# Optimization experiments

Measured on AMD Instinct MI355X. Metric: run time of the kernel, lower is better.

The kernel has to match this reference:

```python
import jax, jax.numpy as jnp
import numpy as np

N_NODES = 512      # num_nodes (seq_len for LSTM, also output side length)
B = 64             # graph batch -> total nodes = B * N_NODES
T = B * N_NODES    # 32768 total nodes
E = 1048576        # edges before self-loops
D_IN = 128
H = 128
L = 2              # lstm layers


def setup_inputs() -> dict:
    key = jax.random.key(0)
    ks = jax.random.split(key, 12)
    x = jax.random.normal(ks[0], (T, D_IN), dtype=jnp.float32)
    edge_index = jax.random.randint(ks[1], (2, E), 0, T, dtype=jnp.int64)
    edge_weight = jax.random.uniform(ks[2], (E,), dtype=jnp.float32)
    batch = jax.random.randint(ks[3], (T,), 0, B, dtype=jnp.int64)
    s = 1.0 / np.sqrt(H)
    W_gcn = jax.random.normal(ks[4], (D_IN, H), dtype=jnp.float32) * s
    b_gcn = jnp.zeros((H,), dtype=jnp.float32)
    w_ih = jax.random.uniform(ks[5], (L, 4 * H, H), minval=-s, maxval=s, dtype=jnp.float32)
    w_hh = jax.random.uniform(ks[6], (L, 4 * H, H), minval=-s, maxval=s, dtype=jnp.float32)
    b_ih = jax.random.uniform(ks[7], (L, 4 * H), minval=-s, maxval=s, dtype=jnp.float32)
    b_hh = jax.random.uniform(ks[8], (L, 4 * H), minval=-s, maxval=s, dtype=jnp.float32)
    fc_w = jax.random.uniform(ks[9], (N_NODES * N_NODES, H), minval=-s, maxval=s, dtype=jnp.float32)
    fc_b = jax.random.uniform(ks[10], (N_NODES * N_NODES,), minval=-s, maxval=s, dtype=jnp.float32)
    return {"x": x, "edge_index": edge_index, "edge_weight": edge_weight, "batch": batch,
            "W_gcn": W_gcn, "b_gcn": b_gcn, "w_ih": w_ih, "w_hh": w_hh,
            "b_ih": b_ih, "b_hh": b_hh, "fc_w": fc_w, "fc_b": fc_b}


def _gcn_conv(x, edge_index, edge_weight, W, b):
    # PyG GCNConv with edge weights: add self-loops (w=1), symmetric norm, then aggregate.
    n = x.shape[0]
    loop = jnp.arange(n, dtype=edge_index.dtype)
    src = jnp.concatenate([edge_index[0], loop])
    dst = jnp.concatenate([edge_index[1], loop])
    w = jnp.concatenate([edge_weight, jnp.ones((n,), dtype=edge_weight.dtype)])
    deg = jax.ops.segment_sum(w, dst, num_segments=n)
    dinv = jnp.where(deg > 0, jax.lax.rsqrt(jnp.maximum(deg, 1e-30)), 0.0)
    norm = dinv[src] * w * dinv[dst]                  # [E+n]
    xw = x @ W                                        # [n, H]
    msg = norm[:, None] * xw[src]                     # gather + scale
    out = jax.ops.segment_sum(msg, dst, num_segments=n)  # scatter-add
    return out + b


def _lstm_layer(xs, wih, whh, bih, bhh):
    # xs: [S, B, H] time-major; torch gate order i,f,g,o.
    h0 = jnp.zeros((xs.shape[1], whh.shape[1]), dtype=xs.dtype)
    c0 = jnp.zeros_like(h0)
    def step(carry, xt):
        h, c = carry
        gates = xt @ wih.T + h @ whh.T + bih + bhh
        i, f, g, o = jnp.split(gates, 4, axis=-1)
        c = jax.nn.sigmoid(f) * c + jax.nn.sigmoid(i) * jnp.tanh(g)
        h = jax.nn.sigmoid(o) * jnp.tanh(c)
        return (h, c), h
    _, hs = jax.lax.scan(step, (h0, c0), xs)
    return hs


def reference(x, edge_index, edge_weight, batch, W_gcn, b_gcn, w_ih, w_hh, b_ih, b_hh, fc_w, fc_b):
    h = _gcn_conv(x, edge_index, edge_weight, W_gcn, b_gcn)   # [T, H]
    # split into chunks of num_nodes and stack -> [B, N_NODES, H]
    h = h.reshape(B, N_NODES, H)
    xs = jnp.transpose(h, (1, 0, 2))                           # [S, B, H]
    for l in range(L):
        xs = _lstm_layer(xs, w_ih[l], w_hh[l], b_ih[l], b_hh[l])
    last = xs[-1]                                              # [B, H]
    out = last @ fc_w.T + fc_b                                 # [B, N_NODES^2]
    return out.reshape(N_NODES, -1)
```

## Files before the change

### kernel.cpp

```cpp
#include <hip/hip_runtime.h>

#define TNODES 32768
#define NEDGE  1048576
#define HD     128
#define NG     512
#define NB     64
#define SEQ    512
#define FCN    262144

__global__ __launch_bounds__(256) void k_deg(const int* __restrict__ ei,
                                             const float* __restrict__ ew,
                                             float* __restrict__ deg,
                                             int* __restrict__ cnt) {
    int e = blockIdx.x * 256 + threadIdx.x;
    int d = ei[NEDGE + e];
    atomicAdd(&deg[d], ew[e]);
    atomicAdd(&cnt[d], 1);
}

__global__ __launch_bounds__(256) void k_dinv(float* __restrict__ deg) {
    int n = blockIdx.x * 256 + threadIdx.x;
    deg[n] = rsqrtf(deg[n] + 1.0f);
}

__global__ __launch_bounds__(1024) void k_scan(const int* __restrict__ cnt,
                                               int* __restrict__ offs) {
    __shared__ int sums[1024];
    int t = threadIdx.x;
    int base = t * 32;
    int local[32];
    int s = 0;
    #pragma unroll
    for (int j = 0; j < 32; ++j) { local[j] = s; s += cnt[base + j]; }
    sums[t] = s;
    __syncthreads();
    for (int off = 1; off < 1024; off <<= 1) {
        int v = sums[t];
        int u = (t >= off) ? sums[t - off] : 0;
        __syncthreads();
        sums[t] = v + u;
        __syncthreads();
    }
    int baseSum = (t == 0) ? 0 : sums[t - 1];
    #pragma unroll
    for (int j = 0; j < 32; ++j) offs[base + j] = baseSum + local[j];
    if (t == 1023) offs[TNODES] = sums[1023];
}

__global__ __launch_bounds__(256) void k_fill(const int* __restrict__ ei,
                                              const float* __restrict__ ew,
                                              const float* __restrict__ dinv,
                                              const int* __restrict__ offs,
                                              int* __restrict__ cursor,
                                              int* __restrict__ csrc,
                                              float* __restrict__ ca) {
    int e = blockIdx.x * 256 + threadIdx.x;
    int s = ei[e];
    int d = ei[NEDGE + e];
    int p = offs[d] + atomicAdd(&cursor[d], 1);
    csrc[p] = s;
    ca[p] = ew[e] * dinv[s];
}

__global__ __launch_bounds__(256) void k_transpose(const float* __restrict__ W,
                                                   float* __restrict__ Wt) {
    int t = blockIdx.x * 256 + threadIdx.x;
    int c = t >> 7, k = t & 127;
    Wt[t] = W[k * HD + c];
}

#define GS 140
__global__ __launch_bounds__(256) void k_gemm_bt(const float* __restrict__ A,
                                                 const float* __restrict__ Bt,
                                                 const float* __restrict__ b1,
                                                 const float* __restrict__ b2,
                                                 float* __restrict__ C, int G) {
    __shared__ __align__(16) float As[64 * GS];
    __shared__ __align__(16) float Bs[64 * GS];
    int r0 = blockIdx.x * 64;
    int g0 = blockIdx.y * 64;
    int tid = threadIdx.x;
    #pragma unroll
    for (int it = 0; it < 8; ++it) {
        int idx = tid + 256 * it;
        int r = idx >> 5, c4 = idx & 31;
        float4 va = ((const float4*)(A + (size_t)(r0 + r) * HD))[c4];
        *((float4*)&As[r * GS + c4 * 4]) = va;
        float4 vb = ((const float4*)(Bt + (size_t)(g0 + r) * HD))[c4];
        *((float4*)&Bs[r * GS + c4 * 4]) = vb;
    }
    __syncthreads();
    int i = tid >> 4;
    int j = tid & 15;
    float acc[4][4];
    #pragma unroll
    for (int a = 0; a < 4; ++a)
        #pragma unroll
        for (int b = 0; b < 4; ++b) acc[a][b] = 0.f;
    #pragma unroll 8
    for (int k4 = 0; k4 < 32; ++k4) {
        float4 av[4], bv[4];
        #pragma unroll
        for (int mi = 0; mi < 4; ++mi)
            av[mi] = *((const float4*)&As[(i + 16 * mi) * GS + k4 * 4]);
        #pragma unroll
        for (int ni = 0; ni < 4; ++ni)
            bv[ni] = *((const float4*)&Bs[(j + 16 * ni) * GS + k4 * 4]);
        #pragma unroll
        for (int mi = 0; mi < 4; ++mi)
            #pragma unroll
            for (int ni = 0; ni < 4; ++ni)
                acc[mi][ni] += (av[mi].x * bv[ni].x + av[mi].y * bv[ni].y) +
                               (av[mi].z * bv[ni].z + av[mi].w * bv[ni].w);
    }
    #pragma unroll
    for (int mi = 0; mi < 4; ++mi)
        #pragma unroll
        for (int ni = 0; ni < 4; ++ni) {
            int g = g0 + j + 16 * ni;
            float bias = (b1 ? b1[g] : 0.f) + (b2 ? b2[g] : 0.f);
            C[(size_t)(r0 + i + 16 * mi) * G + g] = acc[mi][ni] + bias;
        }
}

__global__ __launch_bounds__(128) void k_agg(const int* __restrict__ offs,
                                             const int* __restrict__ csrc,
                                             const float* __restrict__ ca,
                                             const float* __restrict__ xw,
                                             const float* __restrict__ dinv,
                                             const float* __restrict__ bg,
                                             float* __restrict__ hg) {
    int d = blockIdx.x;
    int t = threadIdx.x;
    int beg = offs[d], end = offs[d + 1];
    float acc = 0.f;
    int e = beg;
    for (; e + 3 < end; e += 4) {
        int s0 = csrc[e], s1 = csrc[e + 1], s2 = csrc[e + 2], s3 = csrc[e + 3];
        float a0 = ca[e], a1 = ca[e + 1], a2 = ca[e + 2], a3 = ca[e + 3];
        acc += a0 * xw[(size_t)s0 * HD + t];
        acc += a1 * xw[(size_t)s1 * HD + t];
        acc += a2 * xw[(size_t)s2 * HD + t];
        acc += a3 * xw[(size_t)s3 * HD + t];
    }
    for (; e < end; ++e) acc += ca[e] * xw[(size_t)csrc[e] * HD + t];
    float di = dinv[d];
    hg[(size_t)d * HD + t] = di * acc + di * di * xw[(size_t)d * HD + t] + bg[t];
}

__device__ __forceinline__ float sigm(float x) { return 1.f / (1.f + __expf(-x)); }
__device__ __forceinline__ float tanh_s(float x) {
    float e = __expf(-2.f * fabsf(x));
    float t = (1.f - e) / (1.f + e);
    return copysignf(t, x);
}

__global__ __launch_bounds__(512, 2) void k_lstm(const float* __restrict__ P,
                                                 const float* __restrict__ whh,
                                                 float* __restrict__ Hout,
                                                 float* __restrict__ lastOut) {
    __shared__ __align__(16) float h_sh[HD];
    __shared__ float g_sh[NG];
    int b = blockIdx.x, t = threadIdx.x;
    float4 w[32];
    #pragma unroll
    for (int kk = 0; kk < 32; ++kk) w[kk] = ((const float4*)(whh + (size_t)t * HD))[kk];
    float c = 0.f;
    if (t < HD) h_sh[t] = 0.f;
    __syncthreads();
    const float* Pb = P + (size_t)b * SEQ * NG;
    for (int s = 0; s < SEQ; ++s) {
        float p = Pb[(size_t)s * NG + t];
        float a0 = 0.f, a1 = 0.f, a2 = 0.f, a3 = 0.f;
        #pragma unroll
        for (int kk = 0; kk < 32; ++kk) {
            float4 h4 = ((const float4*)h_sh)[kk];
            a0 += w[kk].x * h4.x;
            a1 += w[kk].y * h4.y;
            a2 += w[kk].z * h4.z;
            a3 += w[kk].w * h4.w;
        }
        float raw = ((a0 + a1) + (a2 + a3)) + p;
        float act = (t >= 256 && t < 384) ? tanh_s(raw) : sigm(raw);
        g_sh[t] = act;
        __syncthreads();
        if (t < HD) {
            float i_ = g_sh[t], f_ = g_sh[HD + t], gg = g_sh[2 * HD + t], o_ = g_sh[3 * HD + t];
            c = f_ * c + i_ * gg;
            float h = o_ * tanh_s(c);
            h_sh[t] = h;
            if (Hout) Hout[((size_t)b * SEQ + s) * HD + t] = h;
            if (lastOut && s == SEQ - 1) lastOut[b * HD + t] = h;
        }
        __syncthreads();
    }
}

__global__ __launch_bounds__(256) void k_fc(const float* __restrict__ last,
                                            const float* __restrict__ fcw,
                                            const float* __restrict__ fcb,
                                            float* __restrict__ out) {
    __shared__ __align__(16) float l_sh[NB * HD];
    int tid = threadIdx.x;
    #pragma unroll
    for (int it = 0; it < 32; ++it) l_sh[tid + 256 * it] = last[tid + 256 * it];
    __syncthreads();
    int i = blockIdx.x * 256 + tid;
    const float4* wrow = (const float4*)(fcw + (size_t)i * HD);
    float acc[NB];
    #pragma unroll
    for (int b = 0; b < NB; ++b) acc[b] = 0.f;
    for (int k4 = 0; k4 < 32; ++k4) {
        float4 w4 = wrow[k4];
        #pragma unroll
        for (int b = 0; b < NB; ++b) {
            float4 l4 = ((const float4*)(l_sh + b * HD))[k4];
            acc[b] += (w4.x * l4.x + w4.y * l4.y) + (w4.z * l4.z + w4.w * l4.w);
        }
    }
    float bias = fcb[i];
    #pragma unroll
    for (int b = 0; b < NB; ++b) out[(size_t)b * FCN + i] = acc[b] + bias;
}

extern "C" void kernel_launch(void* const* d_in, const int* in_sizes, int n_in,
                              void* d_out, int out_size, void* d_ws, size_t ws_size,
                              hipStream_t stream) {
    const float* x   = (const float*)d_in[0];
    const int*   ei  = (const int*)d_in[1];
    const float* ew  = (const float*)d_in[2];
    const float* Wg  = (const float*)d_in[4];
    const float* bg  = (const float*)d_in[5];
    const float* wih = (const float*)d_in[6];
    const float* whh = (const float*)d_in[7];
    const float* bih = (const float*)d_in[8];
    const float* bhh = (const float*)d_in[9];
    const float* fcw = (const float*)d_in[10];
    const float* fcb = (const float*)d_in[11];
    float* out = (float*)d_out;

    float* ws = (float*)d_ws;
    float* deg    = ws;
    int*   cnt    = (int*)(ws + 32768);
    int*   cursor = (int*)(ws + 65536);
    int*   offs   = (int*)(ws + 98304);
    int*   csrc   = (int*)(ws + 131136);
    float* ca     = ws + 1179712;
    float* Wt     = ws + 2228288;
    float* xw     = ws + 2244672;
    float* hg     = ws + 6438976;
    float* H0     = ws + 10633280;
    float* lastb  = ws + 14827584;
    float* P      = ws + 14835776;

    hipMemsetAsync(d_ws, 0, 3 * 32768 * sizeof(float), stream);

    k_deg<<<NEDGE / 256, 256, 0, stream>>>(ei, ew, deg, cnt);
    k_dinv<<<TNODES / 256, 256, 0, stream>>>(deg);
    k_scan<<<1, 1024, 0, stream>>>(cnt, offs);
    k_fill<<<NEDGE / 256, 256, 0, stream>>>(ei, ew, deg, offs, cursor, csrc, ca);
    k_transpose<<<64, 256, 0, stream>>>(Wg, Wt);
    k_gemm_bt<<<dim3(TNODES / 64, HD / 64), 256, 0, stream>>>(x, Wt, nullptr, nullptr, xw, HD);
    k_agg<<<TNODES, 128, 0, stream>>>(offs, csrc, ca, xw, deg, bg, hg);

    k_gemm_bt<<<dim3(TNODES / 64, NG / 64), 256, 0, stream>>>(hg, wih, bih, bhh, P, NG);
    k_lstm<<<NB, 512, 0, stream>>>(P, whh, H0, nullptr);
    k_gemm_bt<<<dim3(TNODES / 64, NG / 64), 256, 0, stream>>>(H0, wih + 65536, bih + 512, bhh + 512, P, NG);
    k_lstm<<<NB, 512, 0, stream>>>(P, whh + 65536, nullptr, lastb);

    k_fc<<<FCN / 256, 256, 0, stream>>>(lastb, fcw, fcb, out);
}
```

Baseline: 1.705 ms.

## Restructure LSTM recurrence: two gate rows per thread, readlane broadcast of h

The LSTM kernel now runs 256 threads per block, and each thread holds two rows of the recurrent weight matrix in registers (256 VGPRs of weights). The hidden state is broadcast across the wavefront with readlane instead of being read from shared memory each step. The next step's P input is prefetched one iteration ahead. This is meant to cut LDS traffic and load latency in the serial 512-step recurrence, at the risk of register spills and lower parallelism per block.

```diff
diff --git a/kernel.cpp b/kernel.cpp
--- a/kernel.cpp
+++ b/kernel.cpp
@@ -155,44 +155,76 @@
     return copysignf(t, x);
 }
 
-__global__ __launch_bounds__(512, 2) void k_lstm(const float* __restrict__ P,
+#define COMP(v, j) ((j) == 0 ? (v).x : ((j) == 1 ? (v).y : ((j) == 2 ? (v).z : (v).w)))
+
+__global__ __launch_bounds__(256, 1) void k_lstm(const float* __restrict__ P,
                                                  const float* __restrict__ whh,
                                                  float* __restrict__ Hout,
                                                  float* __restrict__ lastOut) {
     __shared__ __align__(16) float h_sh[HD];
     __shared__ float g_sh[NG];
     int b = blockIdx.x, t = threadIdx.x;
-    float4 w[32];
-    #pragma unroll
-    for (int kk = 0; kk < 32; ++kk) w[kk] = ((const float4*)(whh + (size_t)t * HD))[kk];
+    int lane = t & 63;
+
+    float4 wA[32], wB[32];
+    const float4* rowA = (const float4*)(whh + (size_t)t * HD);
+    const float4* rowB = (const float4*)(whh + (size_t)(t + 256) * HD);
+    #pragma unroll
+    for (int k = 0; k < 32; ++k) { wA[k] = rowA[k]; wB[k] = rowB[k]; }
+    #pragma unroll
+    for (int k = 0; k < 32; ++k) {
+        asm volatile("" : "+v"(wA[k].x), "+v"(wA[k].y), "+v"(wA[k].z), "+v"(wA[k].w));
+        asm volatile("" : "+v"(wB[k].x), "+v"(wB[k].y), "+v"(wB[k].z), "+v"(wB[k].w));
+    }
+
     float c = 0.f;
     if (t < HD) h_sh[t] = 0.f;
     __syncthreads();
+
     const float* Pb = P + (size_t)b * SEQ * NG;
+    float p0 = Pb[t], p1 = Pb[256 + t];
+
     for (int s = 0; s < SEQ; ++s) {
-        float p = Pb[(size_t)s * NG + t];
-        float a0 = 0.f, a1 = 0.f, a2 = 0.f, a3 = 0.f;
-        #pragma unroll
-        for (int kk = 0; kk < 32; ++kk) {
-            float4 h4 = ((const float4*)h_sh)[kk];
-            a0 += w[kk].x * h4.x;
-            a1 += w[kk].y * h4.y;
-            a2 += w[kk].z * h4.z;
-            a3 += w[kk].w * h4.w;
-        }
-        float raw = ((a0 + a1) + (a2 + a3)) + p;
-        float act = (t >= 256 && t < 384) ? tanh_s(raw) : sigm(raw);
-        g_sh[t] = act;
+        const float* Pn = Pb + (size_t)((s + 1 < SEQ) ? (s + 1) : s) * NG;
+        float q0 = Pn[t], q1 = Pn[256 + t];
+
+        float hv0 = h_sh[lane];
+        float hv1 = h_sh[64 + lane];
+
+        float accA[4] = {0.f, 0.f, 0.f, 0.f};
+        float accB[4] = {0.f, 0.f, 0.f, 0.f};
+        #pragma unroll
+        for (int k = 0; k < 64; ++k) {
+            float h = __int_as_float(__builtin_amdgcn_readlane(__float_as_int(hv0), k));
+            accA[k & 3] = fmaf(COMP(wA[k >> 2], k & 3), h, accA[k & 3]);
+            accB[k & 3] = fmaf(COMP(wB[k >> 2], k & 3), h, accB[k & 3]);
+        }
+        #pragma unroll
+        for (int k = 0; k < 64; ++k) {
+            float h = __int_as_float(__builtin_amdgcn_readlane(__float_as_int(hv1), k));
+            accA[k & 3] = fmaf(COMP(wA[16 + (k >> 2)], k & 3), h, accA[k & 3]);
+            accB[k & 3] = fmaf(COMP(wB[16 + (k >> 2)], k & 3), h, accB[k & 3]);
+        }
+        float rawA = ((accA[0] + accA[1]) + (accA[2] + accA[3])) + p0;
+        float rawB = ((accB[0] + accB[1]) + (accB[2] + accB[3])) + p1;
+
+        float gA = sigm(rawA);
+        float gB = (t < 128) ? tanh_s(rawB) : sigm(rawB);
+        g_sh[t] = gA;
+        g_sh[256 + t] = gB;
         __syncthreads();
+
         if (t < HD) {
-            float i_ = g_sh[t], f_ = g_sh[HD + t], gg = g_sh[2 * HD + t], o_ = g_sh[3 * HD + t];
-            c = f_ * c + i_ * gg;
+            float i_ = g_sh[t], f_ = g_sh[128 + t], gg = g_sh[256 + t], o_ = g_sh[384 + t];
+            c = fmaf(f_, c, i_ * gg);
             float h = o_ * tanh_s(c);
             h_sh[t] = h;
             if (Hout) Hout[((size_t)b * SEQ + s) * HD + t] = h;
             if (lastOut && s == SEQ - 1) lastOut[b * HD + t] = h;
         }
         __syncthreads();
+        p0 = q0;
+        p1 = q1;
     }
 }
 
@@ -264,9 +296,9 @@
     k_agg<<<TNODES, 128, 0, stream>>>(offs, csrc, ca, xw, deg, bg, hg);
 
     k_gemm_bt<<<dim3(TNODES / 64, NG / 64), 256, 0, stream>>>(hg, wih, bih, bhh, P, NG);
-    k_lstm<<<NB, 512, 0, stream>>>(P, whh, H0, nullptr);
+    k_lstm<<<NB, 256, 0, stream>>>(P, whh, H0, nullptr);
     k_gemm_bt<<<dim3(TNODES / 64, NG / 64), 256, 0, stream>>>(H0, wih + 65536, bih + 512, bhh + 512, P, NG);
-    k_lstm<<<NB, 512, 0, stream>>>(P, whh + 65536, nullptr, lastb);
+    k_lstm<<<NB, 256, 0, stream>>>(P, whh + 65536, nullptr, lastb);
 
     k_fc<<<FCN / 256, 256, 0, stream>>>(lastb, fcw, fcb, out);
 }
```

Measured after the change: 2.299 ms. 34.8% more time.

## Repartition LSTM recurrence so each thread handles four gates over a K-slice

Applied to the files above, without the earlier changes.

The LSTM recurrent matvec is restructured. Each thread now holds weights for all four gates of one hidden unit over a 32-wide K chunk, transposed through LDS at load time. Hidden values are broadcast with readlane instead of per-thread float4 LDS reads, and partial sums are written as float4 and reduced by the first 128 threads, which also apply the gate activations. The next step's input projections are prefetched into registers. This cuts LDS read traffic per step and moves the activations onto fewer threads, at the cost of a reduction pass and a larger shared buffer.

```diff
diff --git a/kernel.cpp b/kernel.cpp
--- a/kernel.cpp
+++ b/kernel.cpp
@@ -155,42 +155,79 @@
     return copysignf(t, x);
 }
 
+#define COMP(v, j) ((j) == 0 ? (v).x : ((j) == 1 ? (v).y : ((j) == 2 ? (v).z : (v).w)))
+
 __global__ __launch_bounds__(512, 2) void k_lstm(const float* __restrict__ P,
                                                  const float* __restrict__ whh,
                                                  float* __restrict__ Hout,
                                                  float* __restrict__ lastOut) {
-    __shared__ __align__(16) float h_sh[HD];
-    __shared__ float g_sh[NG];
+    __shared__ __align__(16) float lds[18560];
+    float* h_sh = lds + 18432;
     int b = blockIdx.x, t = threadIdx.x;
-    float4 w[32];
-    #pragma unroll
-    for (int kk = 0; kk < 32; ++kk) w[kk] = ((const float4*)(whh + (size_t)t * HD))[kk];
-    float c = 0.f;
+    int c = t >> 7;
+    int i = t & 127;
+
+    float4 w[4][8];
+    for (int cc = 0; cc < 4; ++cc) {
+        const float4* src = (const float4*)(whh + (size_t)t * HD + 32 * cc);
+        float4 tmp[8];
+        #pragma unroll
+        for (int q = 0; q < 8; ++q) tmp[q] = src[q];
+        __syncthreads();
+        #pragma unroll
+        for (int q = 0; q < 8; ++q)
+            *((float4*)(lds + t * 36 + 4 * q)) = tmp[q];
+        __syncthreads();
+        if (cc == c) {
+            #pragma unroll
+            for (int g = 0; g < 4; ++g)
+                #pragma unroll
+                for (int q = 0; q < 8; ++q)
+                    w[g][q] = *((const float4*)(lds + (i + 128 * g) * 36 + 4 * q));
+        }
+    }
+    __syncthreads();
+
     if (t < HD) h_sh[t] = 0.f;
-    __syncthreads();
+    float cst = 0.f;
     const float* Pb = P + (size_t)b * SEQ * NG;
+    float pi = 0.f, pf = 0.f, pg = 0.f, po = 0.f;
+    if (t < HD) { pi = Pb[t]; pf = Pb[128 + t]; pg = Pb[256 + t]; po = Pb[384 + t]; }
+    __syncthreads();
+
     for (int s = 0; s < SEQ; ++s) {
-        float p = Pb[(size_t)s * NG + t];
-        float a0 = 0.f, a1 = 0.f, a2 = 0.f, a3 = 0.f;
-        #pragma unroll
-        for (int kk = 0; kk < 32; ++kk) {
-            float4 h4 = ((const float4*)h_sh)[kk];
-            a0 += w[kk].x * h4.x;
-            a1 += w[kk].y * h4.y;
-            a2 += w[kk].z * h4.z;
-            a3 += w[kk].w * h4.w;
-        }
-        float raw = ((a0 + a1) + (a2 + a3)) + p;
-        float act = (t >= 256 && t < 384) ? tanh_s(raw) : sigm(raw);
-        g_sh[t] = act;
-        __syncthreads();
+        float hv = h_sh[32 * c + (t & 31)];
+        float4 acc = {0.f, 0.f, 0.f, 0.f};
+        #pragma unroll
+        for (int k = 0; k < 32; ++k) {
+            float h = __int_as_float(__builtin_amdgcn_readlane(__float_as_int(hv), k));
+            acc.x = fmaf(COMP(w[0][k >> 2], k & 3), h, acc.x);
+            acc.y = fmaf(COMP(w[1][k >> 2], k & 3), h, acc.y);
+            acc.z = fmaf(COMP(w[2][k >> 2], k & 3), h, acc.z);
+            acc.w = fmaf(COMP(w[3][k >> 2], k & 3), h, acc.w);
+        }
+        ((float4*)lds)[c * 128 + i] = acc;
+        __syncthreads();
+
         if (t < HD) {
-            float i_ = g_sh[t], f_ = g_sh[HD + t], gg = g_sh[2 * HD + t], o_ = g_sh[3 * HD + t];
-            c = f_ * c + i_ * gg;
-            float h = o_ * tanh_s(c);
+            float4 s0 = ((const float4*)lds)[t];
+            float4 s1 = ((const float4*)lds)[128 + t];
+            float4 s2 = ((const float4*)lds)[256 + t];
+            float4 s3 = ((const float4*)lds)[384 + t];
+            float gi = (s0.x + s1.x) + (s2.x + s3.x) + pi;
+            float gf = (s0.y + s1.y) + (s2.y + s3.y) + pf;
+            float gg = (s0.z + s1.z) + (s2.z + s3.z) + pg;
+            float go = (s0.w + s1.w) + (s2.w + s3.w) + po;
+            float i_ = sigm(gi), f_ = sigm(gf), g_ = tanh_s(gg), o_ = sigm(go);
+            cst = fmaf(f_, cst, i_ * g_);
+            float h = o_ * tanh_s(cst);
             h_sh[t] = h;
             if (Hout) Hout[((size_t)b * SEQ + s) * HD + t] = h;
             if (lastOut && s == SEQ - 1) lastOut[b * HD + t] = h;
+            if (s + 1 < SEQ) {
+                const float* Pn = Pb + (size_t)(s + 1) * NG;
+                pi = Pn[t]; pf = Pn[128 + t]; pg = Pn[256 + t]; po = Pn[384 + t];
+            }
         }
         __syncthreads();
     }
```

New measurement: 1.675 ms. Within noise of the previous version (-1.8%).
